# Kernel optimization log

Hardware: AMD Instinct MI355X
Metric: run time of the kernel (lower is better)

## Reference

```python
import jax, jax.numpy as jnp
import numpy as np

N_NODES = 50000
N_EDGES = 800000
D_IN = 128
D_OUT = 128


def setup_inputs() -> dict:
    key = jax.random.key(0)
    ks = jax.random.split(key, 6)
    x = jax.random.normal(ks[0], (N_NODES, D_IN), dtype=jnp.float32)
    edge_src = jax.random.randint(ks[1], (N_EDGES,), 0, N_NODES)
    edge_dst = jax.random.randint(ks[2], (N_EDGES,), 0, N_NODES)
    edge_val = jax.random.uniform(ks[3], (N_EDGES,), dtype=jnp.float32)
    W = jax.random.normal(ks[4], (D_OUT, D_IN), dtype=jnp.float32) / np.sqrt(D_IN)
    b = jax.random.normal(ks[5], (D_OUT,), dtype=jnp.float32) * 0.01
    return {"x": x, "edge_src": edge_src, "edge_dst": edge_dst,
            "edge_val": edge_val, "W": W, "b": b}


def reference(x, edge_src, edge_dst, edge_val, W, b):
    # h = sparse.mm(adj, x): for each edge (dst, src, val): h[dst] += val * x[src]
    msgs = edge_val[:, None] * x[edge_src]            # [E, D_IN]
    h = jax.ops.segment_sum(msgs, edge_dst, num_segments=N_NODES)  # [N, D_IN]
    # nn.Linear: h @ W.T + b, then relu activation
    out = jnp.einsum('nd,od->no', h, W) + b           # [N, D_OUT]
    return jax.nn.relu(out)
```

## Files before the change

### kernel.cpp

```cpp
#include <hip/hip_runtime.h>
#include <hip/hip_bf16.h>

#define N_NODES 50000
#define N_EDGES 800000
#define D 128
#define SCAN_NB 49

typedef __attribute__((ext_vector_type(8))) short short8;
typedef __attribute__((ext_vector_type(4))) float f32x4;
typedef unsigned int uint;
typedef unsigned short ushort;

__device__ __forceinline__ ushort f2bf(float f) {
    uint u = __float_as_uint(f);
    u += 0x7fffu + ((u >> 16) & 1u);
    return (ushort)(u >> 16);
}


__global__ __launch_bounds__(256) void sgcn_prep(
    const float* __restrict__ W, ushort* __restrict__ Wb, int* __restrict__ deg)
{
    int t = blockIdx.x * 256 + threadIdx.x;
    if (t < (D * D) / 4) {
        float4 a = reinterpret_cast<const float4*>(W)[t];
        ushort4 s;
        s.x = f2bf(a.x); s.y = f2bf(a.y); s.z = f2bf(a.z); s.w = f2bf(a.w);
        *reinterpret_cast<ushort4*>(Wb + (size_t)t * 4) = s;
    }
    if (t < N_NODES / 4) {
        reinterpret_cast<int4*>(deg)[t] = make_int4(0, 0, 0, 0);
    }
}


__global__ __launch_bounds__(256) void sgcn_hist_rank(
    const int* __restrict__ dst, int* __restrict__ deg, int* __restrict__ rank)
{
    int e = blockIdx.x * 256 + threadIdx.x;
    if (e < N_EDGES)
        rank[e] = atomicAdd(&deg[dst[e]], 1);
}

__global__ __launch_bounds__(256) void sgcn_scan1(
    const int* __restrict__ deg, int* __restrict__ blockSum)
{
    __shared__ int red[256];
    int tid = threadIdx.x;
    int base = blockIdx.x * 1024 + tid * 4;
    int4 v = make_int4(0, 0, 0, 0);
    if (base < N_NODES) v = *reinterpret_cast<const int4*>(deg + base);
    red[tid] = v.x + v.y + v.z + v.w;
    __syncthreads();
    for (int off = 128; off > 0; off >>= 1) {
        if (tid < off) red[tid] += red[tid + off];
        __syncthreads();
    }
    if (tid == 0) blockSum[blockIdx.x] = red[0];
}

__global__ __launch_bounds__(256) void sgcn_scan3f(
    const int* __restrict__ deg, const int* __restrict__ blockSum,
    int* __restrict__ rowptr)
{
    __shared__ int part[256];
    __shared__ int off0;
    int tid = threadIdx.x;
    if (tid < 64) {
        int v = (tid < blockIdx.x) ? blockSum[tid] : 0;
#pragma unroll
        for (int o = 32; o > 0; o >>= 1) v += __shfl_down(v, o);
        if (tid == 0) off0 = v;
    }
    int base = blockIdx.x * 1024 + tid * 4;
    int4 v = make_int4(0, 0, 0, 0);
    if (base < N_NODES) v = *reinterpret_cast<const int4*>(deg + base);
    int s = v.x + v.y + v.z + v.w;
    part[tid] = s;
    __syncthreads();
    for (int off = 1; off < 256; off <<= 1) {
        int mine  = part[tid];
        int other = (tid >= off) ? part[tid - off] : 0;
        __syncthreads();
        part[tid] = mine + other;
        __syncthreads();
    }
    int run = off0 + ((tid == 0) ? 0 : part[tid - 1]);
    if (base < N_NODES) {
        int4 r;
        r.x = run;
        r.y = run + v.x;
        r.z = r.y + v.y;
        r.w = r.z + v.z;
        *reinterpret_cast<int4*>(rowptr + base) = r;
        if (base + 4 == N_NODES) rowptr[N_NODES] = r.w + v.w;
    }
}

__global__ __launch_bounds__(256) void sgcn_permute(
    const int* __restrict__ src, const int* __restrict__ dst,
    const float* __restrict__ val, const int* __restrict__ rowptr,
    const int* __restrict__ rank, int2* __restrict__ epair)
{
    int e = blockIdx.x * 256 + threadIdx.x;
    if (e < N_EDGES) {
        int pos = rowptr[dst[e]] + rank[e];
        int2 p;
        p.x = src[e];
        p.y = __float_as_int(val[e]);
        epair[pos] = p;
    }
}


__global__ __launch_bounds__(256) void sgcn_gemm_y(
    const float* __restrict__ x, const ushort* __restrict__ Wb,
    ushort* __restrict__ y)
{
    int wave = threadIdx.x >> 6;
    int lane = threadIdx.x & 63;
    int lm = lane & 15;
    int kb = lane >> 4;

    short8 bfr[8][4];
#pragma unroll
    for (int nt = 0; nt < 8; ++nt)
#pragma unroll
        for (int kk = 0; kk < 4; ++kk)
            bfr[nt][kk] = *reinterpret_cast<const short8*>(
                Wb + (nt * 16 + lm) * D + kk * 32 + kb * 8);

    const int nMT = N_NODES / 16;
    int mt0 = blockIdx.x * 4 + wave;
    int strideMT = gridDim.x * 4;
    for (int mt = mt0; mt < nMT; mt += strideMT) {
        int m0 = mt * 16;
        const float* xrow = x + (long)(m0 + lm) * D + kb * 8;
        short8 afr[4];
#pragma unroll
        for (int kk = 0; kk < 4; ++kk) {
            float4 a = *reinterpret_cast<const float4*>(xrow + kk * 32);
            float4 c = *reinterpret_cast<const float4*>(xrow + kk * 32 + 4);
            short8 s;
            s[0] = (short)f2bf(a.x); s[1] = (short)f2bf(a.y);
            s[2] = (short)f2bf(a.z); s[3] = (short)f2bf(a.w);
            s[4] = (short)f2bf(c.x); s[5] = (short)f2bf(c.y);
            s[6] = (short)f2bf(c.z); s[7] = (short)f2bf(c.w);
            afr[kk] = s;
        }
#pragma unroll
        for (int nt = 0; nt < 8; ++nt) {
            f32x4 acc = {0.f, 0.f, 0.f, 0.f};
#pragma unroll
            for (int kk = 0; kk < 4; ++kk)
                acc = __builtin_amdgcn_mfma_f32_16x16x32_bf16(afr[kk], bfr[nt][kk], acc, 0, 0, 0);
            ushort* yp = y + (long)(m0 + kb * 4) * D + nt * 16 + lm;
#pragma unroll
            for (int r = 0; r < 4; ++r)
                yp[(long)r * D] = f2bf(acc[r]);
        }
    }
}


__device__ __forceinline__ float bflo(uint u) { return __uint_as_float(u << 16); }
__device__ __forceinline__ float bfhi(uint u) { return __uint_as_float(u & 0xffff0000u); }

__global__ __launch_bounds__(256) void sgcn_aggregate(
    const uint* __restrict__ yb, const int* __restrict__ rowptr,
    const int2* __restrict__ epair, const float* __restrict__ bias,
    float* __restrict__ out)
{
    int gw   = (blockIdx.x * 256 + threadIdx.x) >> 6;
    int lane = threadIdx.x & 63;
    int nW   = (gridDim.x * 256) >> 6;
    float2 bv = *reinterpret_cast<const float2*>(bias + lane * 2);
    for (int n = gw; n < N_NODES; n += nW) {
        int j0 = rowptr[n], j1 = rowptr[n + 1];
        float ax = 0.f, ay = 0.f;
        int j = j0;
        for (; j + 8 <= j1; j += 8) {
#pragma unroll
            for (int q = 0; q < 8; ++q) {
                int2 p = epair[j + q];
                uint u = yb[(long)p.x * 64 + lane];
                float v = __int_as_float(p.y);
                ax += v * bflo(u);
                ay += v * bfhi(u);
            }
        }
        for (; j < j1; ++j) {
            int2 p = epair[j];
            uint u = yb[(long)p.x * 64 + lane];
            float v = __int_as_float(p.y);
            ax += v * bflo(u);
            ay += v * bfhi(u);
        }
        float2 r;
        r.x = fmaxf(ax + bv.x, 0.f);
        r.y = fmaxf(ay + bv.y, 0.f);
        *reinterpret_cast<float2*>(out + (long)n * D + lane * 2) = r;
    }
}

extern "C" void kernel_launch(void* const* d_in, const int* in_sizes, int n_in,
                              void* d_out, int out_size, void* d_ws, size_t ws_size,
                              hipStream_t stream) {
    const float* x   = (const float*)d_in[0];
    const int*   es  = (const int*)d_in[1];
    const int*   ed  = (const int*)d_in[2];
    const float* ev  = (const float*)d_in[3];
    const float* W   = (const float*)d_in[4];
    const float* b   = (const float*)d_in[5];
    float* out = (float*)d_out;

    char* ws = (char*)d_ws;
    size_t off = 0;
    uint*   yb       = (uint*)  (ws + off); off += (size_t)N_NODES * (D / 2) * sizeof(uint);
    ushort* Wb       = (ushort*)(ws + off); off += (size_t)D * D * sizeof(ushort);
    int2*   epair    = (int2*)  (ws + off); off += (size_t)N_EDGES * sizeof(int2);
    int*    rowptr   = (int*)   (ws + off); off += ((size_t)(N_NODES + 1) * sizeof(int) + 15) & ~15ull;
    int*    deg      = (int*)   (ws + off); off += (size_t)N_NODES * sizeof(int);
    int*    blockSum = (int*)   (ws + off); off += 64 * sizeof(int);
    int* rank = (int*)d_out;

    const int EB = (N_EDGES + 255) / 256;

    sgcn_prep<<<64, 256, 0, stream>>>(W, Wb, deg);
    sgcn_gemm_y<<<512, 256, 0, stream>>>(x, Wb, (ushort*)yb);
    sgcn_hist_rank<<<EB, 256, 0, stream>>>(ed, deg, rank);
    sgcn_scan1<<<SCAN_NB, 256, 0, stream>>>(deg, blockSum);
    sgcn_scan3f<<<SCAN_NB, 256, 0, stream>>>(deg, blockSum, rowptr);
    sgcn_permute<<<EB, 256, 0, stream>>>(es, ed, ev, rowptr, rank, epair);
    sgcn_aggregate<<<2048, 256, 0, stream>>>(yb, rowptr, epair, b, out);
}
```

Before: 118.7 us.

## Pack edges into 32-bit words and split aggregation into two column-half passes

Each edge's source index and bf16 value are packed into one 32-bit word, halving the edge stream. Aggregation now runs twice, once per 64-column half of y. In each pass the two half-waves handle alternate edges, and the halves are combined with a cross-lane shuffle. The two passes are meant to shrink each pass's gather working set for better cache locality, at the cost of reading the edge list and rowptr twice and rounding edge weights to bf16.

```diff
diff --git a/kernel.cpp b/kernel.cpp
--- a/kernel.cpp
+++ b/kernel.cpp
@@ -5,6 +5,8 @@
 #define N_EDGES 800000
 #define D 128
 #define SCAN_NB 49
+
+static_assert(N_NODES < 65536, "src must fit in 16 bits for epack");
 
 typedef __attribute__((ext_vector_type(8))) short short8;
 typedef __attribute__((ext_vector_type(4))) float f32x4;
@@ -100,15 +102,12 @@
 __global__ __launch_bounds__(256) void sgcn_permute(
     const int* __restrict__ src, const int* __restrict__ dst,
     const float* __restrict__ val, const int* __restrict__ rowptr,
-    const int* __restrict__ rank, int2* __restrict__ epair)
+    const int* __restrict__ rank, uint* __restrict__ epack)
 {
     int e = blockIdx.x * 256 + threadIdx.x;
     if (e < N_EDGES) {
         int pos = rowptr[dst[e]] + rank[e];
-        int2 p;
-        p.x = src[e];
-        p.y = __float_as_int(val[e]);
-        epair[pos] = p;
+        epack[pos] = ((uint)f2bf(val[e]) << 16) | (uint)src[e];
     }
 }
 
@@ -166,40 +165,50 @@
 __device__ __forceinline__ float bflo(uint u) { return __uint_as_float(u << 16); }
 __device__ __forceinline__ float bfhi(uint u) { return __uint_as_float(u & 0xffff0000u); }
 
+template<int PASS>
 __global__ __launch_bounds__(256) void sgcn_aggregate(
     const uint* __restrict__ yb, const int* __restrict__ rowptr,
-    const int2* __restrict__ epair, const float* __restrict__ bias,
+    const uint* __restrict__ ep, const float* __restrict__ bias,
     float* __restrict__ out)
 {
     int gw   = (blockIdx.x * 256 + threadIdx.x) >> 6;
     int lane = threadIdx.x & 63;
+    int h    = lane >> 5;
+    int l    = lane & 31;
     int nW   = (gridDim.x * 256) >> 6;
-    float2 bv = *reinterpret_cast<const float2*>(bias + lane * 2);
+    float2 bv = *reinterpret_cast<const float2*>(bias + PASS * 64 + 2 * l);
     for (int n = gw; n < N_NODES; n += nW) {
         int j0 = rowptr[n], j1 = rowptr[n + 1];
         float ax = 0.f, ay = 0.f;
         int j = j0;
-        for (; j + 8 <= j1; j += 8) {
-#pragma unroll
-            for (int q = 0; q < 8; ++q) {
-                int2 p = epair[j + q];
-                uint u = yb[(long)p.x * 64 + lane];
-                float v = __int_as_float(p.y);
+        for (; j + 4 <= j1; j += 4) {
+            uint p0 = ep[j + h];
+            uint p1 = ep[j + 2 + h];
+            uint u0 = yb[(long)(p0 & 0xffffu) * 64 + PASS * 32 + l];
+            uint u1 = yb[(long)(p1 & 0xffffu) * 64 + PASS * 32 + l];
+            float v0 = __uint_as_float(p0 & 0xffff0000u);
+            float v1 = __uint_as_float(p1 & 0xffff0000u);
+            ax += v0 * bflo(u0) + v1 * bflo(u1);
+            ay += v0 * bfhi(u0) + v1 * bfhi(u1);
+        }
+        for (; j < j1; j += 2) {
+            int jj = j + h;
+            if (jj < j1) {
+                uint p = ep[jj];
+                uint u = yb[(long)(p & 0xffffu) * 64 + PASS * 32 + l];
+                float v = __uint_as_float(p & 0xffff0000u);
                 ax += v * bflo(u);
                 ay += v * bfhi(u);
             }
         }
-        for (; j < j1; ++j) {
-            int2 p = epair[j];
-            uint u = yb[(long)p.x * 64 + lane];
-            float v = __int_as_float(p.y);
-            ax += v * bflo(u);
-            ay += v * bfhi(u);
-        }
-        float2 r;
-        r.x = fmaxf(ax + bv.x, 0.f);
-        r.y = fmaxf(ay + bv.y, 0.f);
-        *reinterpret_cast<float2*>(out + (long)n * D + lane * 2) = r;
+        ax += __shfl_xor(ax, 32);
+        ay += __shfl_xor(ay, 32);
+        if (h == 0) {
+            float2 r;
+            r.x = fmaxf(ax + bv.x, 0.f);
+            r.y = fmaxf(ay + bv.y, 0.f);
+            *reinterpret_cast<float2*>(out + (long)n * D + PASS * 64 + 2 * l) = r;
+        }
     }
 }
 
@@ -218,7 +227,7 @@
     size_t off = 0;
     uint*   yb       = (uint*)  (ws + off); off += (size_t)N_NODES * (D / 2) * sizeof(uint);
     ushort* Wb       = (ushort*)(ws + off); off += (size_t)D * D * sizeof(ushort);
-    int2*   epair    = (int2*)  (ws + off); off += (size_t)N_EDGES * sizeof(int2);
+    uint*   epack    = (uint*)  (ws + off); off += (size_t)N_EDGES * sizeof(uint);
     int*    rowptr   = (int*)   (ws + off); off += ((size_t)(N_NODES + 1) * sizeof(int) + 15) & ~15ull;
     int*    deg      = (int*)   (ws + off); off += (size_t)N_NODES * sizeof(int);
     int*    blockSum = (int*)   (ws + off); off += 64 * sizeof(int);
@@ -231,6 +240,7 @@
     sgcn_hist_rank<<<EB, 256, 0, stream>>>(ed, deg, rank);
     sgcn_scan1<<<SCAN_NB, 256, 0, stream>>>(deg, blockSum);
     sgcn_scan3f<<<SCAN_NB, 256, 0, stream>>>(deg, blockSum, rowptr);
-    sgcn_permute<<<EB, 256, 0, stream>>>(es, ed, ev, rowptr, rank, epair);
-    sgcn_aggregate<<<2048, 256, 0, stream>>>(yb, rowptr, epair, b, out);
-}
+    sgcn_permute<<<EB, 256, 0, stream>>>(es, ed, ev, rowptr, rank, epack);
+    sgcn_aggregate<0><<<2048, 256, 0, stream>>>(yb, rowptr, epack, b, out);
+    sgcn_aggregate<1><<<2048, 256, 0, stream>>>(yb, rowptr, epack, b, out);
+}
```

Result: slower. 137.4 us (+15.7%).
